# Kernel optimization log

Measured on AMD Instinct MI355X. Metric: run time of the kernel, lower is better.

## Reference

```python
import jax, jax.numpy as jnp
import numpy as np

DIM = 256; HEADS = 8; HD = 32; WS = 3; LOCAL = WS * WS; SR = 4


def _unfold(x, ws):
    # x: (B, c, H, W) -> (B, c, ws*ws, H*W), zero padding (matches nn.Unfold)
    p = ws // 2
    B, c, H, W = x.shape
    xp = jnp.pad(x, ((0, 0), (0, 0), (p, p), (p, p)))
    pat = jnp.stack([xp[:, :, i:i + H, j:j + W] for i in range(ws) for j in range(ws)], axis=2)
    return pat.reshape(B, c, ws * ws, H * W)


def _l2norm(x):
    return x / jnp.sqrt(jnp.sum(x * x, axis=-1, keepdims=True) + 1e-12)


def setup_inputs():
    key = jax.random.key(0)
    ks = jax.random.split(key, 16)
    B, H, W, C, h, d = 4, 64, 64, DIM, HEADS, HD
    N = H * W; pH, pW = H // SR, W // SR; PL = pH * pW; L = 1024
    s = 0.02
    inp = {}
    inp["x"] = jax.random.normal(ks[0], (B, N, C), jnp.float32)
    inp["relative_coords_table"] = jax.random.uniform(ks[1], (L, 2), jnp.float32, -1.0, 1.0)
    inp["relative_pos_index"] = jax.random.randint(ks[2], (N, PL), 0, L)
    inp["q_w"] = jax.random.normal(ks[3], (C, C), jnp.float32) * s
    inp["q_b"] = jnp.zeros((C,), jnp.float32)
    inp["kv_w"] = jax.random.normal(ks[4], (C, 2 * C), jnp.float32) * s
    inp["kv_b"] = jnp.zeros((2 * C,), jnp.float32)
    inp["temperature"] = jnp.log(jnp.expm1(jnp.ones((h, 1, 1), jnp.float32) / 0.24))
    inp["query_embedding"] = jax.random.normal(ks[5], (h, 1, d), jnp.float32) * s
    inp["sr_w"] = jax.random.normal(ks[6], (C, C), jnp.float32) * s
    inp["sr_b"] = jnp.zeros((C,), jnp.float32)
    inp["norm_g"] = jnp.ones((C,), jnp.float32)
    inp["norm_b"] = jnp.zeros((C,), jnp.float32)
    inp["cpb1_w"] = jax.random.normal(ks[7], (2, 512), jnp.float32) * s
    inp["cpb1_b"] = jnp.zeros((512,), jnp.float32)
    inp["cpb2_w"] = jax.random.normal(ks[8], (512, h), jnp.float32) * s
    inp["cpb2_b"] = jnp.zeros((h,), jnp.float32)
    inp["rpb_local"] = jax.random.normal(ks[9], (h, LOCAL), jnp.float32) * 0.0004
    inp["learnable_tokens"] = jax.random.normal(ks[10], (h, d, LOCAL), jnp.float32) * s
    inp["learnable_bias"] = jnp.zeros((h, 1, LOCAL), jnp.float32)
    inp["proj_w"] = jax.random.normal(ks[11], (C, C), jnp.float32) * s
    inp["proj_b"] = jnp.zeros((C,), jnp.float32)
    inp["H"] = H
    inp["W"] = W
    return inp


def _forward(x, relative_coords_table, relative_pos_index, q_w, q_b, kv_w, kv_b,
             temperature, query_embedding, sr_w, sr_b, norm_g, norm_b,
             cpb1_w, cpb1_b, cpb2_w, cpb2_b, rpb_local, learnable_tokens,
             learnable_bias, proj_w, proj_b, H, W):
    B, N, C = x.shape
    h, d = HEADS, HD
    pH, pW = H // SR, W // SR
    PL = pH * pW

    # static buffers: per-pixel valid-neighbor count, log seq-length scale, padding mask
    uf1 = _unfold(jnp.ones((1, 1, H, W), jnp.float32), WS)[0, 0]   # (LOCAL, N)
    counts = uf1.sum(axis=0)[:, None]                               # (N, 1)
    seq_scale = jnp.log(counts + PL)                                # (N, 1)
    pad_mask = (uf1.T == 0)                                         # (N, LOCAL)

    q = (x @ q_w + q_b).reshape(B, N, h, d).transpose(0, 2, 1, 3)   # (B,h,N,d)
    q_norm = _l2norm(q)
    q_scaled = (q_norm + query_embedding) * jax.nn.softplus(temperature) * seq_scale

    kv = (x @ kv_w + kv_b).reshape(B, N, 2 * h, d).transpose(0, 2, 1, 3)
    k_local, v_local = kv[:, :h], kv[:, h:]                         # (B,h,N,d)

    # --- local branch: sliding-window QK^T + learned relative bias ---
    kn = _l2norm(k_local)
    k_img = kn.transpose(0, 1, 3, 2).reshape(B, h * d, H, W)
    k_uf = _unfold(k_img, WS).reshape(B, h, d, LOCAL, N)            # (B,h,d,l,N)
    attn_local = jnp.einsum('bhnd,bhdln->bhnl', q_scaled, k_uf) + rpb_local[None, :, None, :]
    attn_local = jnp.where(pad_mask[None, None], jnp.float32(-1e9), attn_local)

    # --- pooled global branch ---
    xs = jax.nn.gelu(x @ sr_w + sr_b, approximate=False)            # 1x1 conv + GELU
    xs = xs.reshape(B, pH, SR, pW, SR, C).mean(axis=(2, 4)).reshape(B, PL, C)
    mu = xs.mean(-1, keepdims=True)
    var = ((xs - mu) ** 2).mean(-1, keepdims=True)
    xs = (xs - mu) / jnp.sqrt(var + 1e-5) * norm_g + norm_b         # LayerNorm

    kvp = (xs @ kv_w + kv_b).reshape(B, PL, 2 * h, d).transpose(0, 2, 1, 3)
    k_pool, v_pool = kvp[:, :h], kvp[:, h:]
    kp = _l2norm(k_pool)

    # MLP-generated continuous relative position bias
    t = jax.nn.relu(relative_coords_table @ cpb1_w + cpb1_b) @ cpb2_w + cpb2_b  # (L,h)
    pool_bias = t.T[:, relative_pos_index.reshape(-1)].reshape(h, N, PL)

    attn_pool = jnp.einsum('bhnd,bhpd->bhnp', q_scaled, kp) + pool_bias[None]

    # joint softmax over [local | pool]
    attn = jax.nn.softmax(jnp.concatenate([attn_local, attn_pool], axis=-1), axis=-1)
    attn_local, attn_pool = attn[..., :LOCAL], attn[..., LOCAL:]

    # learnable-token refinement of local weights
    attn_local = jnp.einsum('bhnd,hdl->bhnl', q_norm, learnable_tokens) + learnable_bias[None] + attn_local

    v_img = v_local.transpose(0, 1, 3, 2).reshape(B, h * d, H, W)
    v_uf = _unfold(v_img, WS).reshape(B, h, d, LOCAL, N)            # zero-padded V
    x_local = jnp.einsum('bhnl,bhdln->bhnd', attn_local, v_uf)
    x_pool = jnp.einsum('bhnp,bhpd->bhnd', attn_pool, v_pool)

    out = (x_local + x_pool).transpose(0, 2, 1, 3).reshape(B, N, C)
    return out @ proj_w + proj_b


def reference(x, relative_coords_table, relative_pos_index, q_w, q_b, kv_w, kv_b,
              temperature, query_embedding, sr_w, sr_b, norm_g, norm_b,
              cpb1_w, cpb1_b, cpb2_w, cpb2_b, rpb_local, learnable_tokens,
              learnable_bias, proj_w, proj_b, H, W):
    return _forward(x, relative_coords_table, relative_pos_index, q_w, q_b, kv_w, kv_b,
                    temperature, query_embedding, sr_w, sr_b, norm_g, norm_b,
                    cpb1_w, cpb1_b, cpb2_w, cpb2_b, rpb_local, learnable_tokens,
                    learnable_bias, proj_w, proj_b, H, W)
```

## Files before the change

kernel.cpp:

```cpp
#include <hip/hip_runtime.h>
#include <math.h>

#define B_   4
#define N_   4096
#define C_   256
#define NH   8
#define D_   32
#define PL_  256
#define IMG  64

typedef __attribute__((ext_vector_type(8))) short short8b;
typedef __attribute__((ext_vector_type(4))) float f32x4;
typedef unsigned short ushort_t;

__device__ __forceinline__ ushort_t f2bf(float f) {
    unsigned u = __float_as_uint(f);
    u += 0x7FFFu + ((u >> 16) & 1u);
    return (ushort_t)(u >> 16);
}
__device__ __forceinline__ float bf2f(ushort_t s) {
    return __uint_as_float(((unsigned)s) << 16);
}
__device__ __forceinline__ unsigned pk2(float lo, float hi) {
    return (unsigned)f2bf(lo) | ((unsigned)f2bf(hi) << 16);
}
__device__ __forceinline__ float gelu_f(float v) {
    return 0.5f * v * (1.0f + erff(v * 0.70710678118654752440f));
}

__global__ __launch_bounds__(256) void prep_all(const float* __restrict__ x,
                                                const float* __restrict__ q_w,
                                                const float* __restrict__ kv_w,
                                                const float* __restrict__ sr_w,
                                                const float* __restrict__ p_w,
                                                const float* __restrict__ rct,
                                                const float* __restrict__ c1w,
                                                const float* __restrict__ c1b,
                                                const float* __restrict__ c2w,
                                                const float* __restrict__ c2b,
                                                ushort_t* __restrict__ x_bf,
                                                ushort_t* __restrict__ WTall,
                                                ushort_t* __restrict__ pwT,
                                                float* __restrict__ tT)
{
    const int blk = blockIdx.x;
    const int tid = threadIdx.x;
    if (blk < 2048) {
        int gid = blk * 256 + tid;
        const float4* p = (const float4*)(x + (size_t)gid * 8);
        float4 v0 = p[0], v1 = p[1];
        short8b o;
        o[0]=(short)f2bf(v0.x); o[1]=(short)f2bf(v0.y);
        o[2]=(short)f2bf(v0.z); o[3]=(short)f2bf(v0.w);
        o[4]=(short)f2bf(v1.x); o[5]=(short)f2bf(v1.y);
        o[6]=(short)f2bf(v1.z); o[7]=(short)f2bf(v1.w);
        *(short8b*)&x_bf[(size_t)gid * 8] = o;
    } else if (blk < 2208) {
        int wt = (blk - 2048) * 256 + tid;
        int row = wt >> 5;
        int k0  = (wt & 31) << 3;
        const float* W; int N, n; ushort_t* dst;
        if (row < 256)       { W = q_w;  N = 256; n = row;        dst = WTall + (size_t)row * 256; }
        else if (row < 768)  { W = kv_w; N = 512; n = row - 256;  dst = WTall + (size_t)row * 256; }
        else if (row < 1024) { W = sr_w; N = 256; n = row - 768;  dst = WTall + (size_t)row * 256; }
        else                 { W = p_w;  N = 256; n = row - 1024; dst = pwT + (size_t)(row-1024) * 256; }
        short8b v;
        #pragma unroll
        for (int j = 0; j < 8; ++j) v[j] = (short)f2bf(W[(size_t)(k0 + j) * N + n]);
        *(short8b*)&dst[k0] = v;
    } else {
        int l = (blk - 2208) * 4 + (tid >> 6);
        int lane = tid & 63;
        float c0 = rct[l*2+0], c1 = rct[l*2+1];
        float acc[8] = {0,0,0,0,0,0,0,0};
        for (int j = lane; j < 512; j += 64) {
            float hv = fmaxf(c0 * c1w[j] + c1 * c1w[512+j] + c1b[j], 0.f);
            #pragma unroll
            for (int hh = 0; hh < 8; ++hh) acc[hh] += hv * c2w[j*8 + hh];
        }
        #pragma unroll
        for (int o = 32; o > 0; o >>= 1)
            #pragma unroll
            for (int hh = 0; hh < 8; ++hh) acc[hh] += __shfl_xor(acc[hh], o, 64);
        if (lane < 8) tT[lane * 1024 + l] = acc[lane] + c2b[lane];
    }
}

__global__ __launch_bounds__(256) void gemm_fused(const ushort_t* __restrict__ Abf,
                                                  const ushort_t* __restrict__ WTall,
                                                  const float* __restrict__ q_b,
                                                  const float* __restrict__ kv_b,
                                                  const float* __restrict__ sr_b,
                                                  const float* __restrict__ temp,
                                                  const float* __restrict__ qe,
                                                  const int* __restrict__ rpi,
                                                  const float* __restrict__ tT,
                                                  ushort_t* __restrict__ pbl,
                                                  ushort_t* __restrict__ qs_bf,
                                                  ushort_t* __restrict__ knv_bf,
                                                  float* __restrict__ buf_sr)
{
    __shared__ __align__(16) ushort_t Bs[64 * 256];

    const int tid  = threadIdx.x;

    if (blockIdx.y >= 128) {
        int pbid = (blockIdx.y - 128) * 16 + blockIdx.x;
        int gid = pbid * 256 + tid;
        int la   = gid & 15;
        int lg   = (gid >> 4) & 3;
        int t    = (gid >> 6) & 15;
        int wv   = (gid >> 10) & 3;
        int tile = (gid >> 12) & 63;
        int h    = gid >> 18;
        int n  = tile * 64 + wv * 16 + la;
        int p0 = t * 16 + lg * 4;
        int4 r = *(const int4*)&rpi[(size_t)n * PL_ + p0];
        const float* tTh = tT + h * 1024;
        ushort4 o;
        o.x = f2bf(tTh[r.x]);
        o.y = f2bf(tTh[r.y]);
        o.z = f2bf(tTh[r.z]);
        o.w = f2bf(tTh[r.w]);
        *(ushort4*)&pbl[(size_t)gid * 4] = o;
        return;
    }

    const int wv   = tid >> 6;
    const int lane = tid & 63;
    const int la   = lane & 15, lg = lane >> 4;
    const int m0   = blockIdx.y * 128 + wv * 32;
    const int bx   = blockIdx.x;
    const int n0   = bx * 64;

    {
        const int srow = tid >> 2, sm = tid & 3;
        const ushort_t* wrow = WTall + (size_t)(n0 + srow) * 256;
        #pragma unroll
        for (int c8 = 0; c8 < 8; ++c8) {
            int ck = c8 * 4 + sm;
            short8b v = *(const short8b*)&wrow[ck * 8];
            *(short8b*)&Bs[srow * 256 + ((ck ^ (srow & 3)) * 8)] = v;
        }
    }
    __syncthreads();

    const ushort_t* a0p = Abf + (size_t)(m0 + la) * 256 + lg * 8;
    const ushort_t* a1p = a0p + (size_t)16 * 256;

    f32x4 acc[2][4];
    #pragma unroll
    for (int i = 0; i < 2; ++i)
        #pragma unroll
        for (int j = 0; j < 4; ++j) acc[i][j] = (f32x4){0.f, 0.f, 0.f, 0.f};

    #pragma unroll
    for (int kit = 0; kit < 8; ++kit) {
        short8b a0 = *(const short8b*)(a0p + kit * 32);
        short8b a1 = *(const short8b*)(a1p + kit * 32);
        #pragma unroll
        for (int nf = 0; nf < 4; ++nf) {
            int brow = nf * 16 + la;
            short8b bb = *(const short8b*)&Bs[brow * 256 + (((kit*4 + lg) ^ (la & 3)) * 8)];
            acc[0][nf] = __builtin_amdgcn_mfma_f32_16x16x32_bf16(a0, bb, acc[0][nf], 0, 0, 0);
            acc[1][nf] = __builtin_amdgcn_mfma_f32_16x16x32_bf16(a1, bb, acc[1][nf], 0, 0, 0);
        }
    }

    if (bx < 8) {
        const float* bias = (bx < 4) ? q_b : kv_b;
        const int cb = (bx < 4) ? n0 : (n0 - 256);
        float bv[4];
        #pragma unroll
        for (int nf = 0; nf < 4; ++nf) bv[nf] = bias[cb + nf*16 + la];
        float sp0 = 0.f, sp1 = 0.f;
        if (bx < 4) {
            sp0 = log1pf(expf(temp[bx*2 + 0]));
            sp1 = log1pf(expf(temp[bx*2 + 1]));
        }
        #pragma unroll
        for (int mf = 0; mf < 2; ++mf)
            #pragma unroll
            for (int reg = 0; reg < 4; ++reg) {
                int m = m0 + mf*16 + lg*4 + reg;
                #pragma unroll
                for (int h2 = 0; h2 < 2; ++h2) {
                    float v0 = acc[mf][2*h2][reg]   + bv[2*h2];
                    float v1 = acc[mf][2*h2+1][reg] + bv[2*h2+1];
                    float ss = v0*v0 + v1*v1;
                    ss += __shfl_xor(ss, 1, 64);
                    ss += __shfl_xor(ss, 2, 64);
                    ss += __shfl_xor(ss, 4, 64);
                    ss += __shfl_xor(ss, 8, 64);
                    float inv = rsqrtf(ss + 1e-12f);
                    if (bx < 4) {
                        int head = bx*2 + h2;
                        int n = m & (N_-1);
                        int y = n >> 6, xc = n & 63;
                        int cnt = (1 + (y > 0) + (y < IMG-1)) * (1 + (xc > 0) + (xc < IMG-1));
                        float lc = (cnt == 4) ? 5.5606816f : (cnt == 6) ? 5.5683445f : 5.5797298f;
                        float s2 = (h2 ? sp1 : sp0) * lc;
                        ushort_t* dst = qs_bf + (size_t)m * 256 + head*32;
                        dst[la]      = f2bf((v0*inv + qe[head*32 + la])      * s2);
                        dst[16 + la] = f2bf((v1*inv + qe[head*32 + 16 + la]) * s2);
                    } else {
                        int head = (bx-4)*2 + h2;
                        ushort_t* dst = knv_bf + (size_t)m * 512 + head*32;
                        dst[la]      = f2bf(v0*inv);
                        dst[16 + la] = f2bf(v1*inv);
                    }
                }
            }
    } else if (bx < 12) {
        #pragma unroll
        for (int mf = 0; mf < 2; ++mf)
            #pragma unroll
            for (int nf = 0; nf < 4; ++nf)
                #pragma unroll
                for (int reg = 0; reg < 4; ++reg) {
                    int m = m0 + mf*16 + lg*4 + reg;
                    int col_kv = n0 - 256 + nf*16 + la;
                    knv_bf[(size_t)m * 512 + col_kv] =
                        f2bf(acc[mf][nf][reg] + kv_b[col_kv]);
                }
    } else {
        #pragma unroll
        for (int mf = 0; mf < 2; ++mf)
            #pragma unroll
            for (int nf = 0; nf < 4; ++nf)
                #pragma unroll
                for (int reg = 0; reg < 4; ++reg) {
                    int m = m0 + mf*16 + lg*4 + reg;
                    int c = n0 + nf*16 + la - 768;
                    buf_sr[(size_t)m * 256 + c] = gelu_f(acc[mf][nf][reg] + sr_b[c]);
                }
    }
}

__global__ __launch_bounds__(256) void gemm_kvp(const ushort_t* __restrict__ Abf,
                                                const ushort_t* __restrict__ WT,
                                                const float* __restrict__ kv_b,
                                                ushort_t* __restrict__ kp_bf,
                                                ushort_t* __restrict__ vpT_bf)
{
    __shared__ __align__(16) ushort_t Bs[64 * 256];

    const int tid  = threadIdx.x;
    const int wv   = tid >> 6;
    const int lane = tid & 63;
    const int la   = lane & 15, lg = lane >> 4;
    const int m0   = blockIdx.y * 128 + wv * 32;
    const int bx   = blockIdx.x;
    const int n0   = bx * 64;

    {
        const int srow = tid >> 2, sm = tid & 3;
        const ushort_t* wrow = WT + (size_t)(n0 + srow) * 256;
        #pragma unroll
        for (int c8 = 0; c8 < 8; ++c8) {
            int ck = c8 * 4 + sm;
            short8b v = *(const short8b*)&wrow[ck * 8];
            *(short8b*)&Bs[srow * 256 + ((ck ^ (srow & 3)) * 8)] = v;
        }
    }
    __syncthreads();

    const ushort_t* a0p = Abf + (size_t)(m0 + la) * 256 + lg * 8;
    const ushort_t* a1p = a0p + (size_t)16 * 256;

    f32x4 acc[2][4];
    #pragma unroll
    for (int i = 0; i < 2; ++i)
        #pragma unroll
        for (int j = 0; j < 4; ++j) acc[i][j] = (f32x4){0.f, 0.f, 0.f, 0.f};

    #pragma unroll
    for (int kit = 0; kit < 8; ++kit) {
        short8b a0 = *(const short8b*)(a0p + kit * 32);
        short8b a1 = *(const short8b*)(a1p + kit * 32);
        #pragma unroll
        for (int nf = 0; nf < 4; ++nf) {
            int brow = nf * 16 + la;
            short8b bb = *(const short8b*)&Bs[brow * 256 + (((kit*4 + lg) ^ (la & 3)) * 8)];
            acc[0][nf] = __builtin_amdgcn_mfma_f32_16x16x32_bf16(a0, bb, acc[0][nf], 0, 0, 0);
            acc[1][nf] = __builtin_amdgcn_mfma_f32_16x16x32_bf16(a1, bb, acc[1][nf], 0, 0, 0);
        }
    }

    if (bx < 4) {
        float bv[4];
        #pragma unroll
        for (int nf = 0; nf < 4; ++nf) bv[nf] = kv_b[n0 + nf*16 + la];
        #pragma unroll
        for (int mf = 0; mf < 2; ++mf)
            #pragma unroll
            for (int reg = 0; reg < 4; ++reg) {
                int m = m0 + mf*16 + lg*4 + reg;
                int b = m >> 8, p = m & 255;
                #pragma unroll
                for (int h2 = 0; h2 < 2; ++h2) {
                    float v0 = acc[mf][2*h2][reg]   + bv[2*h2];
                    float v1 = acc[mf][2*h2+1][reg] + bv[2*h2+1];
                    float ss = v0*v0 + v1*v1;
                    ss += __shfl_xor(ss, 1, 64);
                    ss += __shfl_xor(ss, 2, 64);
                    ss += __shfl_xor(ss, 4, 64);
                    ss += __shfl_xor(ss, 8, 64);
                    float inv = rsqrtf(ss + 1e-12f);
                    int head = bx*2 + h2;
                    ushort_t* dst = kp_bf + (((size_t)(b*NH + head)) * PL_ + p) * 32;
                    dst[la]      = f2bf(v0*inv);
                    dst[16 + la] = f2bf(v1*inv);
                }
            }
    } else {
        #pragma unroll
        for (int mf = 0; mf < 2; ++mf)
            #pragma unroll
            for (int nf = 0; nf < 4; ++nf)
                #pragma unroll
                for (int reg = 0; reg < 4; ++reg) {
                    int m = m0 + mf*16 + lg*4 + reg;
                    int b = m >> 8, p = m & 255;
                    int col_kv = n0 + nf*16 + la;
                    int cv = col_kv - 256;
                    int head = cv >> 5, d = cv & 31;
                    vpT_bf[(((size_t)(b*NH + head)) * 32 + d) * 256 + p] =
                        f2bf(acc[mf][nf][reg] + kv_b[col_kv]);
                }
    }
}

template<int ACT>
__global__ __launch_bounds__(256) void gemm_mfma(const ushort_t* __restrict__ Abf,
                                                 const ushort_t* __restrict__ WT,
                                                 const float* __restrict__ bias,
                                                 float* __restrict__ out,
                                                 int M, int N)
{
    __shared__ __align__(16) ushort_t Bs[64 * 256];

    const int tid  = threadIdx.x;
    const int wv   = tid >> 6;
    const int lane = tid & 63;
    const int la   = lane & 15, lg = lane >> 4;
    const int m0   = blockIdx.y * 128 + wv * 32;
    const int n0   = blockIdx.x * 64;

    {
        const int srow = tid >> 2, sm = tid & 3;
        const ushort_t* wrow = WT + (size_t)(n0 + srow) * 256;
        #pragma unroll
        for (int c8 = 0; c8 < 8; ++c8) {
            int ck = c8 * 4 + sm;
            short8b v = *(const short8b*)&wrow[ck * 8];
            *(short8b*)&Bs[srow * 256 + ((ck ^ (srow & 3)) * 8)] = v;
        }
    }
    __syncthreads();

    const ushort_t* a0p = Abf + (size_t)(m0 + la) * 256 + lg * 8;
    const ushort_t* a1p = a0p + (size_t)16 * 256;

    f32x4 acc[2][4];
    #pragma unroll
    for (int i = 0; i < 2; ++i)
        #pragma unroll
        for (int j = 0; j < 4; ++j) acc[i][j] = (f32x4){0.f, 0.f, 0.f, 0.f};

    #pragma unroll
    for (int kit = 0; kit < 8; ++kit) {
        short8b a0 = *(const short8b*)(a0p + kit * 32);
        short8b a1 = *(const short8b*)(a1p + kit * 32);
        #pragma unroll
        for (int nf = 0; nf < 4; ++nf) {
            int brow = nf * 16 + la;
            short8b bb = *(const short8b*)&Bs[brow * 256 + (((kit*4 + lg) ^ (la & 3)) * 8)];
            acc[0][nf] = __builtin_amdgcn_mfma_f32_16x16x32_bf16(a0, bb, acc[0][nf], 0, 0, 0);
            acc[1][nf] = __builtin_amdgcn_mfma_f32_16x16x32_bf16(a1, bb, acc[1][nf], 0, 0, 0);
        }
    }
    #pragma unroll
    for (int mf = 0; mf < 2; ++mf)
        #pragma unroll
        for (int nf = 0; nf < 4; ++nf)
            #pragma unroll
            for (int reg = 0; reg < 4; ++reg) {
                int m  = m0 + mf * 16 + lg * 4 + reg;
                int nn = n0 + nf * 16 + la;
                float v = acc[mf][nf][reg] + bias[nn];
                if (ACT == 1) v = gelu_f(v);
                out[(size_t)m * N + nn] = v;
            }
}

__global__ __launch_bounds__(256) void mid_prep(const ushort_t* __restrict__ knv,
                                                const float* __restrict__ sr,
                                                const float* __restrict__ g,
                                                const float* __restrict__ bb,
                                                ushort_t* __restrict__ xs,
                                                ushort_t* __restrict__ vT)
{
    __shared__ float red[256];
    __shared__ __align__(16) ushort_t ts[256][40];
    const int blk = blockIdx.x;
    const int tid = threadIdx.x;

    if (blk < 1024) {
        int bp = blk;
        int b = bp >> 8, p = bp & 255;
        int i0 = p >> 4, j0 = p & 15;
        int c = tid;
        float s = 0.f;
        #pragma unroll
        for (int di = 0; di < 4; ++di)
            #pragma unroll
            for (int dj = 0; dj < 4; ++dj) {
                int n = (i0*4 + di) * IMG + (j0*4 + dj);
                s += sr[((size_t)b * N_ + n) * C_ + c];
            }
        s *= (1.f / 16.f);
        red[c] = s; __syncthreads();
        for (int o = 128; o > 0; o >>= 1) { if (c < o) red[c] += red[c+o]; __syncthreads(); }
        float mean = red[0] * (1.f/256.f);
        __syncthreads();
        float dcen = s - mean;
        red[c] = dcen * dcen; __syncthreads();
        for (int o = 128; o > 0; o >>= 1) { if (c < o) red[c] += red[c+o]; __syncthreads(); }
        float var = red[0] * (1.f/256.f);
        float outv = dcen * rsqrtf(var + 1e-5f) * g[c] + bb[c];
        xs[(size_t)bp * C_ + c] = f2bf(outv);
    } else {
        int vb = blk - 1024;
        int nt = vb & 15, bh = vb >> 4;
        const ushort_t* src = knv + ((size_t)((bh >> 3)*N_ + nt*256 + tid)) * 512 + 256 + (bh & 7)*32;
        #pragma unroll
        for (int c = 0; c < 4; ++c)
            *(short8b*)&ts[tid][c*8] = *(const short8b*)&src[c*8];
        __syncthreads();
        int d = tid >> 3, cc = tid & 7;
        ushort_t* dst = vT + ((size_t)bh*32 + d) * (size_t)N_ + nt*256;
        #pragma unroll
        for (int k = 0; k < 4; ++k) {
            int n0 = cc*32 + k*8;
            short8b v;
            #pragma unroll
            for (int j = 0; j < 8; ++j) v[j] = ts[n0+j][d];
            *(short8b*)&dst[n0] = v;
        }
    }
}

__global__ __launch_bounds__(256) void attn_v4(
    const ushort_t* __restrict__ qs_g,
    const ushort_t* __restrict__ knv_g,
    const ushort_t* __restrict__ kp_g,
    const ushort_t* __restrict__ vpT_g,
    const ushort_t* __restrict__ vT_g,
    const ushort_t* __restrict__ pbl,
    const float* __restrict__ rpb,
    const float* __restrict__ qe,
    const float* __restrict__ temp,
    const float* __restrict__ lt,
    const float* __restrict__ lb,
    ushort_t* __restrict__ outp)
{
    __shared__ __align__(16) ushort_t qs_lds[64*32];
    __shared__ __align__(16) ushort_t ltT_lds[16*32];
    __shared__ __align__(16) ushort_t Wb_lds[4*3*16*40];
    __shared__ float wloc[64*10];
    __shared__ float wext[64*10];
    __shared__ float invs2[64];
    __shared__ float rpb_lds[9], elb_lds[9];

    const int lin  = blockIdx.x;
    const int virt = (lin & 7) * 256 + (lin >> 3);
    const int tile = virt & 63;
    const int hh   = (virt >> 6) & 7;
    const int b    = virt >> 9;

    const int tid  = threadIdx.x;
    const int wv   = tid >> 6;
    const int lane = tid & 63;
    const int la   = lane & 15;
    const int lg   = lane >> 4;
    const int r0   = wv * 16;

    {
        int row = tid >> 2, ck = tid & 3;
        short8b v = *(const short8b*)&qs_g[((size_t)(b*N_ + tile*64 + row)) * 256 + hh*32 + ck*8];
        *(short8b*)&qs_lds[row*32 + ((ck ^ (row & 3)) * 8)] = v;
    }
    {
        int l = tid >> 4, dd = (tid & 15) * 2;
        ushort_t a = (l < 9) ? f2bf(lt[hh*288 + dd*9 + l]) : (ushort_t)0;
        ushort_t c = (l < 9) ? f2bf(lt[hh*288 + (dd+1)*9 + l]) : (ushort_t)0;
        ltT_lds[l*32 + dd]   = a;
        ltT_lds[l*32 + dd+1] = c;
    }
    {
        short8b z = {0,0,0,0,0,0,0,0};
        for (int i = tid; i < 960; i += 256) *(short8b*)&Wb_lds[i*8] = z;
    }
    if (tid < 64) {
        int xx = tid;
        int ci = 1 + (tile > 0) + (tile < IMG-1);
        int cj = 1 + (xx > 0) + (xx < IMG-1);
        float sp = log1pf(expf(temp[hh]));
        invs2[tid] = 1.0f / (sp * logf((float)(ci*cj) + (float)PL_));
    }
    if (tid >= 64 && tid < 73) {
        int l = tid - 64;
        float e = 0.f;
        for (int d = 0; d < 32; ++d) e += qe[hh*32 + d] * lt[hh*288 + d*9 + l];
        elb_lds[l] = lb[hh*9 + l] - e;
        rpb_lds[l] = rpb[hh*9 + l];
    }
    __syncthreads();

    const short8b af = *(const short8b*)&qs_lds[(r0+la)*32 + ((lg ^ (la & 3)) * 8)];

    {
        f32x4 G[3][2];
        const f32x4 zc = {0.f,0.f,0.f,0.f};
        #pragma unroll
        for (int dyi = 0; dyi < 3; ++dyi) {
            int cy = tile + dyi - 1;
            cy = cy < 0 ? 0 : (cy > 63 ? 63 : cy);
            #pragma unroll
            for (int f = 0; f < 2; ++f) {
                int xp = wv*16 - 8 + 16*f + la;
                xp = xp < 0 ? 0 : (xp > 63 ? 63 : xp);
                const short8b kf = *(const short8b*)
                    &knv_g[((size_t)(b*N_ + cy*64 + xp)) * 512 + hh*32 + lg*8];
                G[dyi][f] = __builtin_amdgcn_mfma_f32_16x16x32_bf16(af, kf, zc, 0, 0, 0);
            }
        }
        #pragma unroll
        for (int f = 0; f < 2; ++f)
            #pragma unroll
            for (int reg = 0; reg < 4; ++reg) {
                int r  = lg*4 + reg;
                int dx = la + 16*f - 8 - r;
                if (dx >= -1 && dx <= 1) {
                    #pragma unroll
                    for (int dyi = 0; dyi < 3; ++dyi)
                        wloc[(r0 + r)*10 + dyi*3 + dx + 1] = G[dyi][f][reg];
                }
            }
    }

    {
        const short8b ltf = *(const short8b*)&ltT_lds[la*32 + lg*8];
        const f32x4 zc = {0.f,0.f,0.f,0.f};
        f32x4 E = __builtin_amdgcn_mfma_f32_16x16x32_bf16(af, ltf, zc, 0, 0, 0);
        if (la < 9) {
            #pragma unroll
            for (int reg = 0; reg < 4; ++reg) {
                int rr = r0 + lg*4 + reg;
                wext[rr*10 + la] = invs2[rr] * E[reg] + elb_lds[la];
            }
        }
    }

    const ushort_t* kph = kp_g + ((size_t)(b*NH + hh) * PL_) * 32;
    const ushort_t* pbw = pbl + ((((size_t)hh * 64 + tile) * 4 + wv) * 4096);

    f32x4 acc[16];
    #pragma unroll
    for (int t = 0; t < 16; ++t) {
        ushort4 b4 = *(const ushort4*)&pbw[t*256 + lg*64 + la*4];
        f32x4 c;
        c[0] = bf2f(b4.x); c[1] = bf2f(b4.y); c[2] = bf2f(b4.z); c[3] = bf2f(b4.w);
        short8b kf = *(const short8b*)&kph[(t*16 + la)*32 + lg*8];
        acc[t] = __builtin_amdgcn_mfma_f32_16x16x32_bf16(kf, af, c, 0, 0, 0);
    }

    const int rr = r0 + la;
    float mx = -3.0e38f;
    #pragma unroll
    for (int t = 0; t < 16; ++t)
        #pragma unroll
        for (int reg = 0; reg < 4; ++reg) mx = fmaxf(mx, acc[t][reg]);
    mx = fmaxf(mx, __shfl_xor(mx, 16, 64));
    mx = fmaxf(mx, __shfl_xor(mx, 32, 64));
    float lv[9];
    #pragma unroll
    for (int l = 0; l < 9; ++l) {
        int dy = l/3 - 1, dx = l%3 - 1;
        int yy = tile + dy, xx = rr + dx;
        bool val = (yy >= 0 && yy < IMG && xx >= 0 && xx < IMG);
        lv[l] = val ? (wloc[rr*10 + l] + rpb_lds[l]) : -1e9f;
        mx = fmaxf(mx, lv[l]);
    }

    float s = 0.f;
    #pragma unroll
    for (int t = 0; t < 16; ++t)
        #pragma unroll
        for (int reg = 0; reg < 4; ++reg) {
            float e = __expf(acc[t][reg] - mx);
            acc[t][reg] = e;
            s += e;
        }
    s += __shfl_xor(s, 16, 64);
    s += __shfl_xor(s, 32, 64);
    float sl = 0.f;
    float el[9];
    #pragma unroll
    for (int l = 0; l < 9; ++l) { el[l] = __expf(lv[l] - mx); sl += el[l]; }
    s += sl;
    const float inv = 1.f / s;

    if (lg == 0) {
        #pragma unroll
        for (int l = 0; l < 9; ++l) {
            int dy = l/3 - 1, dx = l%3 - 1;
            int yy = tile + dy, xx = rr + dx;
            bool val = (yy >= 0 && yy < IMG && xx >= 0 && xx < IMG);
            float wl = el[l]*inv + wext[rr*10 + l];
            Wb_lds[((wv*3 + l/3)*16 + la)*40 + (la + 8 + dx)] =
                val ? f2bf(wl) : (ushort_t)0;
        }
    }

    f32x4 o0 = {0.f,0.f,0.f,0.f}, o1 = {0.f,0.f,0.f,0.f};

    {
        const ushort_t* vTh = vT_g + (size_t)(b*NH + hh) * 32 * N_;
        #pragma unroll
        for (int dyi = 0; dyi < 3; ++dyi) {
            int cy = tile + dyi - 1;
            cy = cy < 0 ? 0 : (cy > 63 ? 63 : cy);
            int nb = cy*64 + wv*16 - 8 + lg*8;
            nb = nb < 0 ? 0 : (nb > (N_ - 8) ? (N_ - 8) : nb);
            short8b wf = *(const short8b*)&Wb_lds[((wv*3 + dyi)*16 + la)*40 + lg*8];
            short8b vf0 = *(const short8b*)&vTh[(size_t)la * N_ + nb];
            short8b vf1 = *(const short8b*)&vTh[(size_t)(16 + la) * N_ + nb];
            o0 = __builtin_amdgcn_mfma_f32_16x16x32_bf16(wf, vf0, o0, 0, 0, 0);
            o1 = __builtin_amdgcn_mfma_f32_16x16x32_bf16(wf, vf1, o1, 0, 0, 0);
        }
    }

    {
        const int src0 = la + 32*(lg & 1);
        const int src1 = src0 + 16;
        const bool hi  = (lg >= 2);
        const ushort_t* vph = vpT_g + ((size_t)(b*NH + hh) * 32) * 256;
        #pragma unroll
        for (int kk = 0; kk < 8; ++kk) {
            unsigned A0 = pk2(acc[2*kk][0]*inv,   acc[2*kk][1]*inv);
            unsigned A1 = pk2(acc[2*kk][2]*inv,   acc[2*kk][3]*inv);
            unsigned B0 = pk2(acc[2*kk+1][0]*inv, acc[2*kk+1][1]*inv);
            unsigned B1 = pk2(acc[2*kk+1][2]*inv, acc[2*kk+1][3]*inv);
            unsigned xa0 = __shfl(A0, src0, 64), xb0 = __shfl(B0, src0, 64);
            unsigned xa1 = __shfl(A1, src0, 64), xb1 = __shfl(B1, src0, 64);
            unsigned ya0 = __shfl(A0, src1, 64), yb0 = __shfl(B0, src1, 64);
            unsigned ya1 = __shfl(A1, src1, 64), yb1 = __shfl(B1, src1, 64);
            union { unsigned u[4]; short8b v; } wf;
            wf.u[0] = hi ? xb0 : xa0;
            wf.u[1] = hi ? xb1 : xa1;
            wf.u[2] = hi ? yb0 : ya0;
            wf.u[3] = hi ? yb1 : ya1;
            short8b vf0 = *(const short8b*)&vph[(size_t)la*256      + kk*32 + lg*8];
            short8b vf1 = *(const short8b*)&vph[(size_t)(16+la)*256 + kk*32 + lg*8];
            o0 = __builtin_amdgcn_mfma_f32_16x16x32_bf16(wf.v, vf0, o0, 0, 0, 0);
            o1 = __builtin_amdgcn_mfma_f32_16x16x32_bf16(wf.v, vf1, o1, 0, 0, 0);
        }
    }

    #pragma unroll
    for (int reg = 0; reg < 4; ++reg) {
        int r2 = r0 + lg*4 + reg;
        int n  = tile*64 + r2;
        ushort_t* orow = outp + ((size_t)(b*N_ + n)) * C_ + hh*32;
        orow[la]      = f2bf(o0[reg]);
        orow[16 + la] = f2bf(o1[reg]);
    }
}

extern "C" void kernel_launch(void* const* d_in, const int* in_sizes, int n_in,
                              void* d_out, int out_size, void* d_ws, size_t ws_size,
                              hipStream_t stream) {
    const float* x    = (const float*)d_in[0];
    const float* rct  = (const float*)d_in[1];
    const int*   rpi  = (const int*)  d_in[2];
    const float* q_w  = (const float*)d_in[3];
    const float* q_b  = (const float*)d_in[4];
    const float* kv_w = (const float*)d_in[5];
    const float* kv_b = (const float*)d_in[6];
    const float* temp = (const float*)d_in[7];
    const float* qe   = (const float*)d_in[8];
    const float* sr_w = (const float*)d_in[9];
    const float* sr_b = (const float*)d_in[10];
    const float* ng   = (const float*)d_in[11];
    const float* nb   = (const float*)d_in[12];
    const float* c1w  = (const float*)d_in[13];
    const float* c1b  = (const float*)d_in[14];
    const float* c2w  = (const float*)d_in[15];
    const float* c2b  = (const float*)d_in[16];
    const float* rpb  = (const float*)d_in[17];
    const float* lt   = (const float*)d_in[18];
    const float* lb   = (const float*)d_in[19];
    const float* p_w  = (const float*)d_in[20];
    const float* p_b  = (const float*)d_in[21];
    float* out = (float*)d_out;

    float* ws = (float*)d_ws;
    const size_t MN = (size_t)B_ * N_;
    float* buf_sr  = ws;
    float* buf_t   = buf_sr + MN * 256;
    ushort_t* x_bf   = (ushort_t*)(buf_t + 8*1024);
    ushort_t* pre_bf = x_bf   + MN * 256;
    ushort_t* WTall  = pre_bf + MN * 256;
    ushort_t* pwT    = WTall  + 1024*256;
    ushort_t* qs_bf  = pwT    + 256*256;
    ushort_t* knv_bf = qs_bf  + MN * 256;
    ushort_t* kp_bf  = knv_bf + MN * 512;
    ushort_t* vpT_bf = kp_bf  + (size_t)B_*NH*PL_*32;
    ushort_t* vT_bf  = vpT_bf + (size_t)B_*NH*32*PL_;
    ushort_t* pbl    = vT_bf  + (size_t)B_*NH*32*N_;
    ushort_t* xs_bf  = pbl    + (size_t)2097152*4;

    const int M = (int)MN;

    prep_all<<<2464, 256, 0, stream>>>(x, q_w, kv_w, sr_w, p_w, rct,
                                       c1w, c1b, c2w, c2b, x_bf, WTall, pwT, buf_t);
    gemm_fused<<<dim3(16, 128 + 512), 256, 0, stream>>>(x_bf, WTall, q_b, kv_b, sr_b,
                                                        temp, qe, rpi, buf_t, pbl,
                                                        qs_bf, knv_bf, buf_sr);
    mid_prep<<<1536, 256, 0, stream>>>(knv_bf, buf_sr, ng, nb, xs_bf, vT_bf);
    gemm_kvp<<<dim3(8, 8), 256, 0, stream>>>(xs_bf, WTall + 256*256, kv_b,
                                             kp_bf, vpT_bf);
    attn_v4<<<2048, 256, 0, stream>>>(qs_bf, knv_bf, kp_bf, vpT_bf, vT_bf,
                                      pbl, rpb, qe, temp, lt, lb, pre_bf);
    gemm_mfma<0><<<dim3(4, M/128), 256, 0, stream>>>(pre_bf, pwT, p_b, out, M, 256);
}
```

Measured before the change: 130.8 us.

## Interleave bias-gather blocks with GEMM blocks and process two tiles per attention block

The fused GEMM kernel now uses a 1D grid where every fifth block runs a GEMM tile and the other four run the position-bias gather. This mixes memory-bound and compute-bound work on the CUs instead of running them as separate grid phases. The attention kernel handles two row tiles per block, so per-head setup (learnable-token transpose, bias terms, softplus) is done once per pair, and it sets a 5-blocks-per-CU launch bound. It also replaces the per-row log computation with hardcoded log(count+256) constants, which ties the code to PL=256 and adds an extra sync per tile.

Result: slower. 212.6 us (+62.5%).

```diff
diff --git a/kernel.cpp b/kernel.cpp
--- a/kernel.cpp
+++ b/kernel.cpp
@@ -102,10 +102,12 @@
 {
     __shared__ __align__(16) ushort_t Bs[64 * 256];
 
-    const int tid  = threadIdx.x;
-
-    if (blockIdx.y >= 128) {
-        int pbid = (blockIdx.y - 128) * 16 + blockIdx.x;
+    const int id  = blockIdx.x;
+    const int tid = threadIdx.x;
+    const int g5  = id / 5;
+
+    if (id - g5 * 5 != 0) {
+        int pbid = id - g5 - 1;
         int gid = pbid * 256 + tid;
         int la   = gid & 15;
         int lg   = (gid >> 4) & 3;
@@ -129,8 +131,8 @@
     const int wv   = tid >> 6;
     const int lane = tid & 63;
     const int la   = lane & 15, lg = lane >> 4;
-    const int m0   = blockIdx.y * 128 + wv * 32;
-    const int bx   = blockIdx.x;
+    const int bx   = g5 & 15;
+    const int m0   = (g5 >> 4) * 128 + wv * 32;
     const int n0   = bx * 64;
 
     {
@@ -451,7 +453,7 @@
     }
 }
 
-__global__ __launch_bounds__(256) void attn_v4(
+__global__ __launch_bounds__(256, 5) void attn_v6(
     const ushort_t* __restrict__ qs_g,
     const ushort_t* __restrict__ knv_g,
     const ushort_t* __restrict__ kp_g,
@@ -470,14 +472,13 @@
     __shared__ __align__(16) ushort_t Wb_lds[4*3*16*40];
     __shared__ float wloc[64*10];
     __shared__ float wext[64*10];
-    __shared__ float invs2[64];
     __shared__ float rpb_lds[9], elb_lds[9];
 
-    const int lin  = blockIdx.x;
-    const int virt = (lin & 7) * 256 + (lin >> 3);
-    const int tile = virt & 63;
-    const int hh   = (virt >> 6) & 7;
-    const int b    = virt >> 9;
+    const int lin   = blockIdx.x;
+    const int virt  = (lin & 7) * 128 + (lin >> 3);
+    const int pairi = virt & 31;
+    const int hh    = (virt >> 5) & 7;
+    const int b     = virt >> 8;
 
     const int tid  = threadIdx.x;
     const int wv   = tid >> 6;
@@ -487,11 +488,6 @@
     const int r0   = wv * 16;
 
     {
-        int row = tid >> 2, ck = tid & 3;
-        short8b v = *(const short8b*)&qs_g[((size_t)(b*N_ + tile*64 + row)) * 256 + hh*32 + ck*8];
-        *(short8b*)&qs_lds[row*32 + ((ck ^ (row & 3)) * 8)] = v;
-    }
-    {
         int l = tid >> 4, dd = (tid & 15) * 2;
         ushort_t a = (l < 9) ? f2bf(lt[hh*288 + dd*9 + l]) : (ushort_t)0;
         ushort_t c = (l < 9) ? f2bf(lt[hh*288 + (dd+1)*9 + l]) : (ushort_t)0;
@@ -502,180 +498,191 @@
         short8b z = {0,0,0,0,0,0,0,0};
         for (int i = tid; i < 960; i += 256) *(short8b*)&Wb_lds[i*8] = z;
     }
-    if (tid < 64) {
-        int xx = tid;
-        int ci = 1 + (tile > 0) + (tile < IMG-1);
-        int cj = 1 + (xx > 0) + (xx < IMG-1);
-        float sp = log1pf(expf(temp[hh]));
-        invs2[tid] = 1.0f / (sp * logf((float)(ci*cj) + (float)PL_));
-    }
-    if (tid >= 64 && tid < 73) {
-        int l = tid - 64;
+    if (tid < 9) {
+        int l = tid;
         float e = 0.f;
         for (int d = 0; d < 32; ++d) e += qe[hh*32 + d] * lt[hh*288 + d*9 + l];
         elb_lds[l] = lb[hh*9 + l] - e;
         rpb_lds[l] = rpb[hh*9 + l];
     }
-    __syncthreads();
-
-    const short8b af = *(const short8b*)&qs_lds[(r0+la)*32 + ((lg ^ (la & 3)) * 8)];
-
-    {
-        f32x4 G[3][2];
-        const f32x4 zc = {0.f,0.f,0.f,0.f};
-        #pragma unroll
-        for (int dyi = 0; dyi < 3; ++dyi) {
-            int cy = tile + dyi - 1;
-            cy = cy < 0 ? 0 : (cy > 63 ? 63 : cy);
-            #pragma unroll
-            for (int f = 0; f < 2; ++f) {
-                int xp = wv*16 - 8 + 16*f + la;
-                xp = xp < 0 ? 0 : (xp > 63 ? 63 : xp);
-                const short8b kf = *(const short8b*)
-                    &knv_g[((size_t)(b*N_ + cy*64 + xp)) * 512 + hh*32 + lg*8];
-                G[dyi][f] = __builtin_amdgcn_mfma_f32_16x16x32_bf16(af, kf, zc, 0, 0, 0);
-            }
-        }
-        #pragma unroll
-        for (int f = 0; f < 2; ++f)
-            #pragma unroll
-            for (int reg = 0; reg < 4; ++reg) {
-                int r  = lg*4 + reg;
-                int dx = la + 16*f - 8 - r;
-                if (dx >= -1 && dx <= 1) {
-                    #pragma unroll
-                    for (int dyi = 0; dyi < 3; ++dyi)
-                        wloc[(r0 + r)*10 + dyi*3 + dx + 1] = G[dyi][f][reg];
+    const float sp = log1pf(expf(temp[hh]));
+    const ushort_t* kph = kp_g + ((size_t)(b*NH + hh) * PL_) * 32;
+    const ushort_t* vph = vpT_g + ((size_t)(b*NH + hh) * 32) * 256;
+    const ushort_t* vTh = vT_g + (size_t)(b*NH + hh) * 32 * N_;
+
+    #pragma unroll 1
+    for (int ti = 0; ti < 2; ++ti) {
+        const int tile = pairi * 2 + ti;
+        if (ti) __syncthreads();
+
+        {
+            int row = tid >> 2, ck = tid & 3;
+            short8b v = *(const short8b*)&qs_g[((size_t)(b*N_ + tile*64 + row)) * 256 + hh*32 + ck*8];
+            *(short8b*)&qs_lds[row*32 + ((ck ^ (row & 3)) * 8)] = v;
+        }
+        __syncthreads();
+
+        const short8b af = *(const short8b*)&qs_lds[(r0+la)*32 + ((lg ^ (la & 3)) * 8)];
+
+        {
+            f32x4 G[3][2];
+            const f32x4 zc = {0.f,0.f,0.f,0.f};
+            #pragma unroll
+            for (int dyi = 0; dyi < 3; ++dyi) {
+                int cy = tile + dyi - 1;
+                cy = cy < 0 ? 0 : (cy > 63 ? 63 : cy);
+                #pragma unroll
+                for (int f = 0; f < 2; ++f) {
+                    int xp = wv*16 - 8 + 16*f + la;
+                    xp = xp < 0 ? 0 : (xp > 63 ? 63 : xp);
+                    const short8b kf = *(const short8b*)
+                        &knv_g[((size_t)(b*N_ + cy*64 + xp)) * 512 + hh*32 + lg*8];
+                    G[dyi][f] = __builtin_amdgcn_mfma_f32_16x16x32_bf16(af, kf, zc, 0, 0, 0);
                 }
             }
-    }
-
-    {
-        const short8b ltf = *(const short8b*)&ltT_lds[la*32 + lg*8];
-        const f32x4 zc = {0.f,0.f,0.f,0.f};
-        f32x4 E = __builtin_amdgcn_mfma_f32_16x16x32_bf16(af, ltf, zc, 0, 0, 0);
-        if (la < 9) {
-            #pragma unroll
-            for (int reg = 0; reg < 4; ++reg) {
-                int rr = r0 + lg*4 + reg;
-                wext[rr*10 + la] = invs2[rr] * E[reg] + elb_lds[la];
-            }
-        }
-    }
-
-    const ushort_t* kph = kp_g + ((size_t)(b*NH + hh) * PL_) * 32;
-    const ushort_t* pbw = pbl + ((((size_t)hh * 64 + tile) * 4 + wv) * 4096);
-
-    f32x4 acc[16];
-    #pragma unroll
-    for (int t = 0; t < 16; ++t) {
-        ushort4 b4 = *(const ushort4*)&pbw[t*256 + lg*64 + la*4];
-        f32x4 c;
-        c[0] = bf2f(b4.x); c[1] = bf2f(b4.y); c[2] = bf2f(b4.z); c[3] = bf2f(b4.w);
-        short8b kf = *(const short8b*)&kph[(t*16 + la)*32 + lg*8];
-        acc[t] = __builtin_amdgcn_mfma_f32_16x16x32_bf16(kf, af, c, 0, 0, 0);
-    }
-
-    const int rr = r0 + la;
-    float mx = -3.0e38f;
-    #pragma unroll
-    for (int t = 0; t < 16; ++t)
-        #pragma unroll
-        for (int reg = 0; reg < 4; ++reg) mx = fmaxf(mx, acc[t][reg]);
-    mx = fmaxf(mx, __shfl_xor(mx, 16, 64));
-    mx = fmaxf(mx, __shfl_xor(mx, 32, 64));
-    float lv[9];
-    #pragma unroll
-    for (int l = 0; l < 9; ++l) {
-        int dy = l/3 - 1, dx = l%3 - 1;
-        int yy = tile + dy, xx = rr + dx;
-        bool val = (yy >= 0 && yy < IMG && xx >= 0 && xx < IMG);
-        lv[l] = val ? (wloc[rr*10 + l] + rpb_lds[l]) : -1e9f;
-        mx = fmaxf(mx, lv[l]);
-    }
-
-    float s = 0.f;
-    #pragma unroll
-    for (int t = 0; t < 16; ++t)
-        #pragma unroll
-        for (int reg = 0; reg < 4; ++reg) {
-            float e = __expf(acc[t][reg] - mx);
-            acc[t][reg] = e;
-            s += e;
-        }
-    s += __shfl_xor(s, 16, 64);
-    s += __shfl_xor(s, 32, 64);
-    float sl = 0.f;
-    float el[9];
-    #pragma unroll
-    for (int l = 0; l < 9; ++l) { el[l] = __expf(lv[l] - mx); sl += el[l]; }
-    s += sl;
-    const float inv = 1.f / s;
-
-    if (lg == 0) {
+            #pragma unroll
+            for (int f = 0; f < 2; ++f)
+                #pragma unroll
+                for (int reg = 0; reg < 4; ++reg) {
+                    int r  = lg*4 + reg;
+                    int dx = la + 16*f - 8 - r;
+                    if (dx >= -1 && dx <= 1) {
+                        #pragma unroll
+                        for (int dyi = 0; dyi < 3; ++dyi)
+                            wloc[(r0 + r)*10 + dyi*3 + dx + 1] = G[dyi][f][reg];
+                    }
+                }
+        }
+
+        {
+            const short8b ltf = *(const short8b*)&ltT_lds[la*32 + lg*8];
+            const f32x4 zc = {0.f,0.f,0.f,0.f};
+            f32x4 E = __builtin_amdgcn_mfma_f32_16x16x32_bf16(af, ltf, zc, 0, 0, 0);
+            if (la < 9) {
+                int ci = 1 + (tile > 0) + (tile < IMG-1);
+                #pragma unroll
+                for (int reg = 0; reg < 4; ++reg) {
+                    int rr = r0 + lg*4 + reg;
+                    int cj = 1 + (rr > 0) + (rr < IMG-1);
+                    int cnt = ci * cj;
+                    float lc = (cnt == 4) ? 5.5606816f : (cnt == 6) ? 5.5683445f : 5.5797298f;
+                    float is2 = 1.0f / (sp * lc);
+                    wext[rr*10 + la] = is2 * E[reg] + elb_lds[la];
+                }
+            }
+        }
+
+        const ushort_t* pbw = pbl + ((((size_t)hh * 64 + tile) * 4 + wv) * 4096);
+
+        f32x4 acc[16];
+        #pragma unroll
+        for (int t = 0; t < 16; ++t) {
+            ushort4 b4 = *(const ushort4*)&pbw[t*256 + lg*64 + la*4];
+            f32x4 c;
+            c[0] = bf2f(b4.x); c[1] = bf2f(b4.y); c[2] = bf2f(b4.z); c[3] = bf2f(b4.w);
+            short8b kf = *(const short8b*)&kph[(t*16 + la)*32 + lg*8];
+            acc[t] = __builtin_amdgcn_mfma_f32_16x16x32_bf16(kf, af, c, 0, 0, 0);
+        }
+
+        const int rr = r0 + la;
+        float mx = -3.0e38f;
+        #pragma unroll
+        for (int t = 0; t < 16; ++t)
+            #pragma unroll
+            for (int reg = 0; reg < 4; ++reg) mx = fmaxf(mx, acc[t][reg]);
+        mx = fmaxf(mx, __shfl_xor(mx, 16, 64));
+        mx = fmaxf(mx, __shfl_xor(mx, 32, 64));
+        float lv[9];
         #pragma unroll
         for (int l = 0; l < 9; ++l) {
             int dy = l/3 - 1, dx = l%3 - 1;
             int yy = tile + dy, xx = rr + dx;
             bool val = (yy >= 0 && yy < IMG && xx >= 0 && xx < IMG);
-            float wl = el[l]*inv + wext[rr*10 + l];
-            Wb_lds[((wv*3 + l/3)*16 + la)*40 + (la + 8 + dx)] =
-                val ? f2bf(wl) : (ushort_t)0;
-        }
-    }
-
-    f32x4 o0 = {0.f,0.f,0.f,0.f}, o1 = {0.f,0.f,0.f,0.f};
-
-    {
-        const ushort_t* vTh = vT_g + (size_t)(b*NH + hh) * 32 * N_;
-        #pragma unroll
-        for (int dyi = 0; dyi < 3; ++dyi) {
-            int cy = tile + dyi - 1;
-            cy = cy < 0 ? 0 : (cy > 63 ? 63 : cy);
-            int nb = cy*64 + wv*16 - 8 + lg*8;
-            nb = nb < 0 ? 0 : (nb > (N_ - 8) ? (N_ - 8) : nb);
-            short8b wf = *(const short8b*)&Wb_lds[((wv*3 + dyi)*16 + la)*40 + lg*8];
-            short8b vf0 = *(const short8b*)&vTh[(size_t)la * N_ + nb];
-            short8b vf1 = *(const short8b*)&vTh[(size_t)(16 + la) * N_ + nb];
-            o0 = __builtin_amdgcn_mfma_f32_16x16x32_bf16(wf, vf0, o0, 0, 0, 0);
-            o1 = __builtin_amdgcn_mfma_f32_16x16x32_bf16(wf, vf1, o1, 0, 0, 0);
-        }
-    }
-
-    {
-        const int src0 = la + 32*(lg & 1);
-        const int src1 = src0 + 16;
-        const bool hi  = (lg >= 2);
-        const ushort_t* vph = vpT_g + ((size_t)(b*NH + hh) * 32) * 256;
-        #pragma unroll
-        for (int kk = 0; kk < 8; ++kk) {
-            unsigned A0 = pk2(acc[2*kk][0]*inv,   acc[2*kk][1]*inv);
-            unsigned A1 = pk2(acc[2*kk][2]*inv,   acc[2*kk][3]*inv);
-            unsigned B0 = pk2(acc[2*kk+1][0]*inv, acc[2*kk+1][1]*inv);
-            unsigned B1 = pk2(acc[2*kk+1][2]*inv, acc[2*kk+1][3]*inv);
-            unsigned xa0 = __shfl(A0, src0, 64), xb0 = __shfl(B0, src0, 64);
-            unsigned xa1 = __shfl(A1, src0, 64), xb1 = __shfl(B1, src0, 64);
-            unsigned ya0 = __shfl(A0, src1, 64), yb0 = __shfl(B0, src1, 64);
-            unsigned ya1 = __shfl(A1, src1, 64), yb1 = __shfl(B1, src1, 64);
-            union { unsigned u[4]; short8b v; } wf;
-            wf.u[0] = hi ? xb0 : xa0;
-            wf.u[1] = hi ? xb1 : xa1;
-            wf.u[2] = hi ? yb0 : ya0;
-            wf.u[3] = hi ? yb1 : ya1;
-            short8b vf0 = *(const short8b*)&vph[(size_t)la*256      + kk*32 + lg*8];
-            short8b vf1 = *(const short8b*)&vph[(size_t)(16+la)*256 + kk*32 + lg*8];
-            o0 = __builtin_amdgcn_mfma_f32_16x16x32_bf16(wf.v, vf0, o0, 0, 0, 0);
-            o1 = __builtin_amdgcn_mfma_f32_16x16x32_bf16(wf.v, vf1, o1, 0, 0, 0);
-        }
-    }
-
-    #pragma unroll
-    for (int reg = 0; reg < 4; ++reg) {
-        int r2 = r0 + lg*4 + reg;
-        int n  = tile*64 + r2;
-        ushort_t* orow = outp + ((size_t)(b*N_ + n)) * C_ + hh*32;
-        orow[la]      = f2bf(o0[reg]);
-        orow[16 + la] = f2bf(o1[reg]);
+            lv[l] = val ? (wloc[rr*10 + l] + rpb_lds[l]) : -1e9f;
+            mx = fmaxf(mx, lv[l]);
+        }
+
+        float s = 0.f;
+        #pragma unroll
+        for (int t = 0; t < 16; ++t)
+            #pragma unroll
+            for (int reg = 0; reg < 4; ++reg) {
+                float e = __expf(acc[t][reg] - mx);
+                acc[t][reg] = e;
+                s += e;
+            }
+        s += __shfl_xor(s, 16, 64);
+        s += __shfl_xor(s, 32, 64);
+        float sl = 0.f;
+        float el[9];
+        #pragma unroll
+        for (int l = 0; l < 9; ++l) { el[l] = __expf(lv[l] - mx); sl += el[l]; }
+        s += sl;
+        const float inv = 1.f / s;
+
+        if (lg == 0) {
+            #pragma unroll
+            for (int l = 0; l < 9; ++l) {
+                int dy = l/3 - 1, dx = l%3 - 1;
+                int yy = tile + dy, xx = rr + dx;
+                bool val = (yy >= 0 && yy < IMG && xx >= 0 && xx < IMG);
+                float wl = el[l]*inv + wext[rr*10 + l];
+                Wb_lds[((wv*3 + l/3)*16 + la)*40 + (la + 8 + dx)] =
+                    val ? f2bf(wl) : (ushort_t)0;
+            }
+        }
+
+        f32x4 o0 = {0.f,0.f,0.f,0.f}, o1 = {0.f,0.f,0.f,0.f};
+
+        {
+            #pragma unroll
+            for (int dyi = 0; dyi < 3; ++dyi) {
+                int cy = tile + dyi - 1;
+                cy = cy < 0 ? 0 : (cy > 63 ? 63 : cy);
+                int nb = cy*64 + wv*16 - 8 + lg*8;
+                nb = nb < 0 ? 0 : (nb > (N_ - 8) ? (N_ - 8) : nb);
+                short8b wf = *(const short8b*)&Wb_lds[((wv*3 + dyi)*16 + la)*40 + lg*8];
+                short8b vf0 = *(const short8b*)&vTh[(size_t)la * N_ + nb];
+                short8b vf1 = *(const short8b*)&vTh[(size_t)(16 + la) * N_ + nb];
+                o0 = __builtin_amdgcn_mfma_f32_16x16x32_bf16(wf, vf0, o0, 0, 0, 0);
+                o1 = __builtin_amdgcn_mfma_f32_16x16x32_bf16(wf, vf1, o1, 0, 0, 0);
+            }
+        }
+
+        {
+            const int src0 = la + 32*(lg & 1);
+            const int src1 = src0 + 16;
+            const bool hi  = (lg >= 2);
+            #pragma unroll
+            for (int kk = 0; kk < 8; ++kk) {
+                unsigned A0 = pk2(acc[2*kk][0]*inv,   acc[2*kk][1]*inv);
+                unsigned A1 = pk2(acc[2*kk][2]*inv,   acc[2*kk][3]*inv);
+                unsigned B0 = pk2(acc[2*kk+1][0]*inv, acc[2*kk+1][1]*inv);
+                unsigned B1 = pk2(acc[2*kk+1][2]*inv, acc[2*kk+1][3]*inv);
+                unsigned xa0 = __shfl(A0, src0, 64), xb0 = __shfl(B0, src0, 64);
+                unsigned xa1 = __shfl(A1, src0, 64), xb1 = __shfl(B1, src0, 64);
+                unsigned ya0 = __shfl(A0, src1, 64), yb0 = __shfl(B0, src1, 64);
+                unsigned ya1 = __shfl(A1, src1, 64), yb1 = __shfl(B1, src1, 64);
+                union { unsigned u[4]; short8b v; } wf;
+                wf.u[0] = hi ? xb0 : xa0;
+                wf.u[1] = hi ? xb1 : xa1;
+                wf.u[2] = hi ? yb0 : ya0;
+                wf.u[3] = hi ? yb1 : ya1;
+                short8b vf0 = *(const short8b*)&vph[(size_t)la*256      + kk*32 + lg*8];
+                short8b vf1 = *(const short8b*)&vph[(size_t)(16+la)*256 + kk*32 + lg*8];
+                o0 = __builtin_amdgcn_mfma_f32_16x16x32_bf16(wf.v, vf0, o0, 0, 0, 0);
+                o1 = __builtin_amdgcn_mfma_f32_16x16x32_bf16(wf.v, vf1, o1, 0, 0, 0);
+            }
+        }
+
+        #pragma unroll
+        for (int reg = 0; reg < 4; ++reg) {
+            int r2 = r0 + lg*4 + reg;
+            int n  = tile*64 + r2;
+            ushort_t* orow = outp + ((size_t)(b*N_ + n)) * C_ + hh*32;
+            orow[la]      = f2bf(o0[reg]);
+            orow[16 + la] = f2bf(o1[reg]);
+        }
     }
 }
 
@@ -726,13 +733,13 @@
 
     prep_all<<<2464, 256, 0, stream>>>(x, q_w, kv_w, sr_w, p_w, rct,
                                        c1w, c1b, c2w, c2b, x_bf, WTall, pwT, buf_t);
-    gemm_fused<<<dim3(16, 128 + 512), 256, 0, stream>>>(x_bf, WTall, q_b, kv_b, sr_b,
-                                                        temp, qe, rpi, buf_t, pbl,
-                                                        qs_bf, knv_bf, buf_sr);
+    gemm_fused<<<10240, 256, 0, stream>>>(x_bf, WTall, q_b, kv_b, sr_b,
+                                          temp, qe, rpi, buf_t, pbl,
+                                          qs_bf, knv_bf, buf_sr);
     mid_prep<<<1536, 256, 0, stream>>>(knv_bf, buf_sr, ng, nb, xs_bf, vT_bf);
     gemm_kvp<<<dim3(8, 8), 256, 0, stream>>>(xs_bf, WTall + 256*256, kv_b,
                                              kp_bf, vpT_bf);
-    attn_v4<<<2048, 256, 0, stream>>>(qs_bf, knv_bf, kp_bf, vpT_bf, vT_bf,
+    attn_v6<<<1024, 256, 0, stream>>>(qs_bf, knv_bf, kp_bf, vpT_bf, vT_bf,
                                       pbl, rpb, qe, temp, lt, lb, pre_bf);
     gemm_mfma<0><<<dim3(4, M/128), 256, 0, stream>>>(pre_bf, pwT, p_b, out, M, 256);
 }
```
